# Optimization experiments

Measured on AMD Instinct MI355X. Metric: run time of the kernel, lower is better.

The kernel has to match this reference:

```python
import jax, jax.numpy as jnp
import numpy as np

B, S, NX, NH = 4, 1024, 1024, 16
HD = NX // NH  # 64


def setup_inputs() -> dict:
    key = jax.random.key(0)
    k1, k2, k3 = jax.random.split(key, 3)
    return {
        "hidden_states": jax.random.normal(k1, (B, S, NX), dtype=jnp.float32),
        "c_attn_w": jax.random.normal(k2, (NX, 3 * NX), dtype=jnp.float32) * 0.02,
        "c_attn_b": jnp.zeros((3 * NX,), dtype=jnp.float32),
        "c_proj_w": jax.random.normal(k3, (NX, NX), dtype=jnp.float32) * 0.02,
        "c_proj_b": jnp.zeros((NX,), dtype=jnp.float32),
    }


def reference(hidden_states, c_attn_w, c_attn_b, c_proj_w, c_proj_b):
    # Conv1D fused QKV projection: x @ W + b, then split into q,k,v
    qkv = hidden_states @ c_attn_w + c_attn_b  # [B,S,3*NX]
    q, k, v = jnp.split(qkv, 3, axis=-1)
    # split heads -> [B, H, S, D]
    def heads(x):
        return x.reshape(B, S, NH, HD).transpose(0, 2, 1, 3)
    q, k, v = heads(q), heads(k), heads(v)
    # scores: q @ k^T / sqrt(D)  (scale=True; NOTE: no causal mask in this fork)
    w = jnp.einsum("bhqd,bhkd->bhqk", q, k) / jnp.sqrt(jnp.asarray(HD, q.dtype))
    w = jax.nn.softmax(w, axis=-1)
    a = jnp.einsum("bhqk,bhkd->bhqd", w, v)  # [B,H,S,D]
    # merge heads -> [B,S,NX]
    a = a.transpose(0, 2, 1, 3).reshape(B, S, NX)
    # output projection (dropout is identity in eval)
    return a @ c_proj_w + c_proj_b
```

## Files before the change

### kernel.cpp

```cpp
#include <hip/hip_runtime.h>
#include <hip/hip_fp16.h>
#include <cmath>

constexpr int Bb  = 4;
constexpr int Ss  = 1024;
constexpr int NXc = 1024;
constexpr int NHc = 16;
constexpr int HDc = 64;

typedef __bf16    bf16x8 __attribute__((ext_vector_type(8)));
typedef _Float16  f16x8  __attribute__((ext_vector_type(8)));
typedef float     f32x4  __attribute__((ext_vector_type(4)));
typedef unsigned short ushortT;
typedef ushortT ushort8v __attribute__((ext_vector_type(8)));

#define QSCALE 0.18033688011112042f

__device__ __forceinline__ ushortT f2h_bits(float x) {
  return __half_as_ushort(__float2half(x));
}
__device__ __forceinline__ float h2f(ushortT h) {
  return __half2float(__ushort_as_half(h));
}
__device__ __forceinline__ void split_f16(float x, ushortT& hi, ushortT& lo) {
  hi = f2h_bits(x);
  lo = f2h_bits(x - h2f(hi));
}

__device__ __forceinline__ void gll16(const void* g, void* l) {
  __builtin_amdgcn_global_load_lds(
      (const __attribute__((address_space(1))) unsigned int*)g,
      (__attribute__((address_space(3))) unsigned int*)l, 16, 0, 0);
}

__device__ __forceinline__ void drain_vmem() {
  asm volatile("s_waitcnt vmcnt(0)" ::: "memory");
  __builtin_amdgcn_sched_barrier(0);
}

__global__ __launch_bounds__(256) void prep_all(
    const float* __restrict__ hs, const float* __restrict__ aw,
    const float* __restrict__ pw,
    ushortT* __restrict__ hF, ushortT* __restrict__ awT,
    ushortT* __restrict__ pwT)
{
  const int bid = blockIdx.x;
  if (bid < 4096) {
    int i = (bid * 256 + threadIdx.x) * 4;
    float4 v = *reinterpret_cast<const float4*>(&hs[i]);
    *reinterpret_cast<ushort4*>(&hF[i]) =
        make_ushort4(f2h_bits(v.x), f2h_bits(v.y), f2h_bits(v.z), f2h_bits(v.w));
    return;
  }
  __shared__ float tile[32][33];
  const int tx = threadIdx.x & 31, ty = threadIdx.x >> 5;
  if (bid < 7168) {
    const int b2 = bid - 4096;
    const int n0 = (b2 % 96) * 32, k0 = (b2 / 96) * 32;
    #pragma unroll
    for (int i = 0; i < 4; ++i)
      tile[ty + i * 8][tx] = aw[(size_t)(k0 + ty + i * 8) * 3072 + n0 + tx];
    __syncthreads();
    #pragma unroll
    for (int i = 0; i < 4; ++i)
      awT[(size_t)(n0 + ty + i * 8) * 1024 + k0 + tx] = f2h_bits(tile[tx][ty + i * 8]);
  } else {
    const int b2 = bid - 7168;
    const int n0 = (b2 & 31) * 32, k0 = (b2 >> 5) * 32;
    #pragma unroll
    for (int i = 0; i < 4; ++i)
      tile[ty + i * 8][tx] = pw[(size_t)(k0 + ty + i * 8) * 1024 + n0 + tx];
    __syncthreads();
    #pragma unroll
    for (int i = 0; i < 4; ++i)
      pwT[(size_t)(n0 + ty + i * 8) * 1024 + k0 + tx] = f2h_bits(tile[tx][ty + i * 8]);
  }
}

__global__ __launch_bounds__(256) void gemm_f16_qkv(
    const ushortT* __restrict__ A16, const ushortT* __restrict__ B16,
    const float* __restrict__ bias,
    ushortT* __restrict__ Qb, ushortT* __restrict__ Kb,
    ushortT* __restrict__ Vt, int M, int N, int K)
{
  constexpr int BK = 64;
  __shared__ ushortT smem[32768];

  const int t    = threadIdx.x;
  const int lane = t & 63;
  const int w    = t >> 6;
  const int wr   = w >> 1, wc = w & 1;
  const int m0 = blockIdx.y * 128;
  const int n0 = blockIdx.x * 128;
  const int l15 = lane & 15;
  const int g   = lane >> 4;

  const int srow  = w * 32 + (lane >> 3);
  const int sslot = (lane & 7) ^ (lane >> 3);

  f32x4 acc[4][4];
  #pragma unroll
  for (int m = 0; m < 4; ++m)
    #pragma unroll
    for (int n = 0; n < 4; ++n)
      #pragma unroll
      for (int r = 0; r < 4; ++r) acc[m][n][r] = 0.f;

  const ushortT* pA = A16 + (size_t)(m0 + srow) * K + sslot * 8;
  const ushortT* pB = B16 + (size_t)(n0 + srow) * K + sslot * 8;

  auto STAGE = [&](ushortT* buf, int k0) {
    #pragma unroll
    for (int i = 0; i < 4; ++i) {
      const size_t gstep = (size_t)i * 8 * K + k0;
      const int    loff  = (w * 32 + i * 8) * BK;
      gll16(pA + gstep, &buf[loff]);
      gll16(pB + gstep, &buf[8192 + loff]);
    }
  };

  const int arow = wr * 64 + l15;
  const int bcol = wc * 64 + l15;

  auto COMPUTE = [&](const ushortT* buf) {
    const ushortT* sA = buf;
    const ushortT* sB = buf + 8192;
    #pragma unroll
    for (int c = 0; c < 2; ++c) {
      const int slot = c * 4 + g;
      f16x8 af[4], bf[4];
      #pragma unroll
      for (int m = 0; m < 4; ++m) {
        int r   = arow + m * 16;
        int off = r * BK + ((slot ^ (r & 7)) * 8);
        af[m] = *reinterpret_cast<const f16x8*>(&sA[off]);
      }
      #pragma unroll
      for (int n = 0; n < 4; ++n) {
        int r   = bcol + n * 16;
        int off = r * BK + ((slot ^ (r & 7)) * 8);
        bf[n] = *reinterpret_cast<const f16x8*>(&sB[off]);
      }
      #pragma unroll
      for (int m = 0; m < 4; ++m)
        #pragma unroll
        for (int n = 0; n < 4; ++n)
          acc[m][n] = __builtin_amdgcn_mfma_f32_16x16x32_f16(af[m], bf[n], acc[m][n], 0, 0, 0);
    }
  };

  const int nt = K / BK;
  STAGE(&smem[0], 0);
  drain_vmem();
  __syncthreads();
  for (int tt = 0; tt < nt; tt += 2) {
    if (tt + 1 < nt) STAGE(&smem[16384], (tt + 1) * BK);
    COMPUTE(&smem[0]);
    drain_vmem();
    __syncthreads();
    if (tt + 2 < nt) STAGE(&smem[0], (tt + 2) * BK);
    COMPUTE(&smem[16384]);
    drain_vmem();
    __syncthreads();
  }

  const int region = n0 >> 10;
  if (region < 2) {
    #pragma unroll
    for (int n = 0; n < 4; ++n) {
      int col_g = n0 + wc * 64 + n * 16 + l15;
      int colm  = col_g & 1023;
      float bv  = bias[col_g];
      #pragma unroll
      for (int m = 0; m < 4; ++m) {
        int row = m0 + wr * 64 + m * 16 + (g << 2);
        #pragma unroll
        for (int r = 0; r < 4; ++r) {
          float v = acc[m][n][r] + bv;
          if (region == 0)
            Qb[(size_t)(row + r) * 1024 + colm] = f2h_bits(v * QSCALE);
          else
            Kb[(size_t)(row + r) * 1024 + colm] = f2h_bits(v);
        }
      }
    }
  } else {
    ushortT* T = smem;
    #pragma unroll
    for (int n = 0; n < 4; ++n) {
      int cl   = wc * 64 + n * 16 + l15;
      float bv = bias[n0 + cl];
      #pragma unroll
      for (int m = 0; m < 4; ++m) {
        int rl = wr * 64 + m * 16 + (g << 2);
        #pragma unroll
        for (int r = 0; r < 4; ++r)
          T[cl * 136 + rl + r] = f2h_bits(acc[m][n][r] + bv);
      }
    }
    __syncthreads();
    const int c  = t >> 1;
    const int rh = (t & 1) * 64;
    const int nn = (n0 - 2048) + c;
    const int hh = nn >> 6, dd = nn & 63;
    const int bb = m0 >> 10;
    const int sl = (m0 & 1023) + rh;
    size_t vbase = ((size_t)((bb * 16 + hh) * 64 + dd)) * 1024 + sl;
    #pragma unroll
    for (int j = 0; j < 8; ++j) {
      ushort8v v = *reinterpret_cast<const ushort8v*>(&T[c * 136 + rh + j * 8]);
      *reinterpret_cast<ushort8v*>(&Vt[vbase + j * 8]) = v;
    }
  }
}

__global__ __launch_bounds__(256) void gemm_f16p2(
    const ushortT* __restrict__ Ah, const ushortT* __restrict__ Al,
    const ushortT* __restrict__ B16,
    const float* __restrict__ bias, float* __restrict__ C,
    int M, int N, int K)
{
  constexpr int BK = 64;
  __shared__ ushortT smem[3 * 8192];
  ushortT* sAh = smem;
  ushortT* sAl = smem + 8192;
  ushortT* sB  = smem + 16384;

  const int t    = threadIdx.x;
  const int lane = t & 63;
  const int w    = t >> 6;
  const int wr   = w >> 1, wc = w & 1;
  const int m0 = blockIdx.y * 128;
  const int n0 = blockIdx.x * 128;
  const int l15 = lane & 15;
  const int g   = lane >> 4;

  const int srow  = w * 32 + (lane >> 3);
  const int sslot = (lane & 7) ^ (lane >> 3);

  f32x4 acc[4][4];
  #pragma unroll
  for (int m = 0; m < 4; ++m)
    #pragma unroll
    for (int n = 0; n < 4; ++n)
      #pragma unroll
      for (int r = 0; r < 4; ++r) acc[m][n][r] = 0.f;

  const ushortT* pAh = Ah  + (size_t)(m0 + srow) * K + sslot * 8;
  const ushortT* pAl = Al  + (size_t)(m0 + srow) * K + sslot * 8;
  const ushortT* pB  = B16 + (size_t)(n0 + srow) * K + sslot * 8;

  for (int k0 = 0; k0 < K; k0 += BK) {
    #pragma unroll
    for (int i = 0; i < 4; ++i) {
      const size_t gstep = (size_t)i * 8 * K + k0;
      const int    loff  = (w * 32 + i * 8) * BK;
      gll16(pAh + gstep, &sAh[loff]);
      gll16(pAl + gstep, &sAl[loff]);
      gll16(pB  + gstep, &sB[loff]);
    }
    __syncthreads();

    const int arow = wr * 64 + l15;
    const int bcol = wc * 64 + l15;
    #pragma unroll
    for (int c = 0; c < 2; ++c) {
      const int slot = c * 4 + g;
      f16x8 afh[4], afl[4], bf[4];
      #pragma unroll
      for (int m = 0; m < 4; ++m) {
        int r   = arow + m * 16;
        int off = r * BK + ((slot ^ (r & 7)) * 8);
        afh[m] = *reinterpret_cast<const f16x8*>(&sAh[off]);
        afl[m] = *reinterpret_cast<const f16x8*>(&sAl[off]);
      }
      #pragma unroll
      for (int n = 0; n < 4; ++n) {
        int r   = bcol + n * 16;
        int off = r * BK + ((slot ^ (r & 7)) * 8);
        bf[n] = *reinterpret_cast<const f16x8*>(&sB[off]);
      }
      #pragma unroll
      for (int m = 0; m < 4; ++m)
        #pragma unroll
        for (int n = 0; n < 4; ++n) {
          acc[m][n] = __builtin_amdgcn_mfma_f32_16x16x32_f16(afh[m], bf[n], acc[m][n], 0, 0, 0);
          acc[m][n] = __builtin_amdgcn_mfma_f32_16x16x32_f16(afl[m], bf[n], acc[m][n], 0, 0, 0);
        }
    }
    __syncthreads();
  }

  #pragma unroll
  for (int n = 0; n < 4; ++n) {
    int col  = n0 + wc * 64 + n * 16 + l15;
    float bv = bias[col];
    #pragma unroll
    for (int m = 0; m < 4; ++m) {
      int row = m0 + wr * 64 + m * 16 + (g << 2);
      #pragma unroll
      for (int r = 0; r < 4; ++r)
        C[(size_t)(row + r) * N + col] = acc[m][n][r] + bv;
    }
  }
}

__global__ __launch_bounds__(256) void attn_mfma(
    const ushortT* __restrict__ Qb, const ushortT* __restrict__ Kb,
    const ushortT* __restrict__ Vt,
    ushortT* __restrict__ aHi, ushortT* __restrict__ aLo)
{
  __shared__ ushortT sK[64 * 64];
  __shared__ ushortT sV[64 * 64];
  __shared__ ushortT sP[64 * 64];

  const int t    = threadIdx.x;
  const int lane = t & 63;
  const int w    = t >> 6;
  const int bh = blockIdx.x, b = bh >> 4, h = bh & 15;
  const int q0 = blockIdx.y * 64;
  const int l15 = lane & 15;
  const int g   = lane >> 4;

  f16x8 qa[2];
  #pragma unroll
  for (int ks = 0; ks < 2; ++ks) {
    size_t addr = (size_t)(b * 1024 + q0 + w * 16 + l15) * 1024
                  + h * 64 + ks * 32 + g * 8;
    qa[ks] = *reinterpret_cast<const f16x8*>(&Qb[addr]);
  }

  const int srow  = lane >> 3;
  const int sslot = (lane & 7) ^ srow;

  f32x4 O[4];
  float lp[4];
  #pragma unroll
  for (int r = 0; r < 4; ++r) lp[r] = 0.f;
  #pragma unroll
  for (int n = 0; n < 4; ++n)
    #pragma unroll
    for (int r = 0; r < 4; ++r) O[n][r] = 0.f;

  for (int kt = 0; kt < 16; ++kt) {
    const int k0 = kt * 64;
    #pragma unroll
    for (int i = 0; i < 2; ++i) {
      int r = w * 16 + i * 8 + srow;
      gll16(&Kb[(size_t)(b * 1024 + k0 + r) * 1024 + h * 64 + sslot * 8],
            &sK[(w * 16 + i * 8) * 64]);
      gll16(&Vt[((size_t)bh * 64 + r) * 1024 + k0 + sslot * 8],
            &sV[(w * 16 + i * 8) * 64]);
    }
    __syncthreads();

    f32x4 sc[4];
    #pragma unroll
    for (int n = 0; n < 4; ++n)
      #pragma unroll
      for (int r = 0; r < 4; ++r) sc[n][r] = 0.f;

    #pragma unroll
    for (int ks = 0; ks < 2; ++ks) {
      f16x8 kb[4];
      #pragma unroll
      for (int n = 0; n < 4; ++n) {
        int row = n * 16 + l15;
        kb[n] = *reinterpret_cast<const f16x8*>(
            &sK[row * 64 + (((g + ks * 4) ^ (row & 7)) * 8)]);
      }
      #pragma unroll
      for (int n = 0; n < 4; ++n)
        sc[n] = __builtin_amdgcn_mfma_f32_16x16x32_f16(qa[ks], kb[n], sc[n], 0, 0, 0);
    }

    #pragma unroll
    for (int n = 0; n < 4; ++n)
      #pragma unroll
      for (int r = 0; r < 4; ++r) {
        float p = exp2f(sc[n][r]);
        sc[n][r] = p;
        lp[r] += p;
      }

    #pragma unroll
    for (int n = 0; n < 4; ++n)
      #pragma unroll
      for (int r = 0; r < 4; ++r) {
        int prow = w * 16 + g * 4 + r;
        int c    = n * 16 + l15;
        int off2 = prow * 64 + ((((c >> 3) ^ (prow & 7)) << 3) | (c & 7));
        sP[off2] = f2h_bits(sc[n][r]);
      }

    #pragma unroll
    for (int ks = 0; ks < 2; ++ks) {
      f16x8 vb[4], pa;
      #pragma unroll
      for (int n = 0; n < 4; ++n) {
        int rd = n * 16 + l15;
        vb[n] = *reinterpret_cast<const f16x8*>(
            &sV[rd * 64 + (((g + ks * 4) ^ (rd & 7)) * 8)]);
      }
      {
        int pr = w * 16 + l15;
        pa = *reinterpret_cast<const f16x8*>(
            &sP[pr * 64 + (((g + ks * 4) ^ (pr & 7)) * 8)]);
      }
      #pragma unroll
      for (int n = 0; n < 4; ++n)
        O[n] = __builtin_amdgcn_mfma_f32_16x16x32_f16(pa, vb[n], O[n], 0, 0, 0);
    }
    __syncthreads();
  }

  #pragma unroll
  for (int off = 1; off < 16; off <<= 1)
    #pragma unroll
    for (int r = 0; r < 4; ++r)
      lp[r] += __shfl_xor(lp[r], off);

  #pragma unroll
  for (int r = 0; r < 4; ++r) {
    float inv = 1.f / lp[r];
    #pragma unroll
    for (int n = 0; n < 4; ++n) {
      ushortT hi, lo;
      split_f16(O[n][r] * inv, hi, lo);
      size_t off = (size_t)(b * 1024 + q0 + w * 16 + g * 4 + r) * 1024
                   + h * 64 + n * 16 + l15;
      aHi[off] = hi;
      aLo[off] = lo;
    }
  }
}

extern "C" void kernel_launch(void* const* d_in, const int* in_sizes, int n_in,
                              void* d_out, int out_size, void* d_ws, size_t ws_size,
                              hipStream_t stream) {
  const float* hs = (const float*)d_in[0];
  const float* aw = (const float*)d_in[1];
  const float* ab = (const float*)d_in[2];
  const float* pw = (const float*)d_in[3];
  const float* pb = (const float*)d_in[4];
  float* out = (float*)d_out;

  char* ws = (char*)d_ws;
  const int M = Bb * Ss;

  ushortT* hF  = (ushortT*)(ws);
  ushortT* awT = (ushortT*)(ws + ( 8u << 20));
  ushortT* pwT = (ushortT*)(ws + (14u << 20));
  ushortT* Qb  = (ushortT*)(ws + (18u << 20));
  ushortT* Kb  = (ushortT*)(ws + (26u << 20));
  ushortT* Vt  = (ushortT*)(ws + (34u << 20));
  ushortT* xHi = (ushortT*)(ws + (42u << 20));
  ushortT* xLo = (ushortT*)(ws + (50u << 20));

  dim3 blk(256);

  prep_all<<<8192, blk, 0, stream>>>(hs, aw, pw, hF, awT, pwT);
  gemm_f16_qkv<<<dim3(3 * NXc / 128, M / 128), blk, 0, stream>>>(
      hF, awT, ab, Qb, Kb, Vt, M, 3 * NXc, NXc);
  attn_mfma<<<dim3(Bb * NHc, Ss / 64), blk, 0, stream>>>(Qb, Kb, Vt, xHi, xLo);
  gemm_f16p2<<<dim3(NXc / 128, M / 128), blk, 0, stream>>>(
      xHi, xLo, pwT, pb, out, M, NXc, NXc);
}
```

Before: 119.2 us.

## Use single f16 attention output, double-buffer proj GEMM, MFMA row sums

The attention output is no longer split into hi/lo f16 pairs. The output projection GEMM now runs one MFMA per tile instead of two and reads half the A traffic. That GEMM also gains a two-stage LDS double buffer, so the next K-tile is fetched while the current one is computed. Softmax row sums are computed by an extra MFMA against a ones vector instead of scalar adds plus shuffles. The cost is lower precision in the projection input and more LDS per block.

```diff
diff --git a/kernel.cpp b/kernel.cpp
--- a/kernel.cpp
+++ b/kernel.cpp
@@ -18,13 +18,6 @@
 
 __device__ __forceinline__ ushortT f2h_bits(float x) {
   return __half_as_ushort(__float2half(x));
-}
-__device__ __forceinline__ float h2f(ushortT h) {
-  return __half2float(__ushort_as_half(h));
-}
-__device__ __forceinline__ void split_f16(float x, ushortT& hi, ushortT& lo) {
-  hi = f2h_bits(x);
-  lo = f2h_bits(x - h2f(hi));
 }
 
 __device__ __forceinline__ void gll16(const void* g, void* l) {
@@ -214,17 +207,13 @@
   }
 }
 
-__global__ __launch_bounds__(256) void gemm_f16p2(
-    const ushortT* __restrict__ Ah, const ushortT* __restrict__ Al,
-    const ushortT* __restrict__ B16,
+__global__ __launch_bounds__(256) void gemm_f16s(
+    const ushortT* __restrict__ A16, const ushortT* __restrict__ B16,
     const float* __restrict__ bias, float* __restrict__ C,
     int M, int N, int K)
 {
   constexpr int BK = 64;
-  __shared__ ushortT smem[3 * 8192];
-  ushortT* sAh = smem;
-  ushortT* sAl = smem + 8192;
-  ushortT* sB  = smem + 16384;
+  __shared__ ushortT smem[32768];
 
   const int t    = threadIdx.x;
   const int lane = t & 63;
@@ -246,33 +235,34 @@
       #pragma unroll
       for (int r = 0; r < 4; ++r) acc[m][n][r] = 0.f;
 
-  const ushortT* pAh = Ah  + (size_t)(m0 + srow) * K + sslot * 8;
-  const ushortT* pAl = Al  + (size_t)(m0 + srow) * K + sslot * 8;
-  const ushortT* pB  = B16 + (size_t)(n0 + srow) * K + sslot * 8;
-
-  for (int k0 = 0; k0 < K; k0 += BK) {
+  const ushortT* pA = A16 + (size_t)(m0 + srow) * K + sslot * 8;
+  const ushortT* pB = B16 + (size_t)(n0 + srow) * K + sslot * 8;
+
+  auto STAGE = [&](ushortT* buf, int k0) {
     #pragma unroll
     for (int i = 0; i < 4; ++i) {
       const size_t gstep = (size_t)i * 8 * K + k0;
       const int    loff  = (w * 32 + i * 8) * BK;
-      gll16(pAh + gstep, &sAh[loff]);
-      gll16(pAl + gstep, &sAl[loff]);
-      gll16(pB  + gstep, &sB[loff]);
-    }
-    __syncthreads();
-
-    const int arow = wr * 64 + l15;
-    const int bcol = wc * 64 + l15;
+      gll16(pA + gstep, &buf[loff]);
+      gll16(pB + gstep, &buf[8192 + loff]);
+    }
+  };
+
+  const int arow = wr * 64 + l15;
+  const int bcol = wc * 64 + l15;
+
+  auto COMPUTE = [&](const ushortT* buf) {
+    const ushortT* sA = buf;
+    const ushortT* sB = buf + 8192;
     #pragma unroll
     for (int c = 0; c < 2; ++c) {
       const int slot = c * 4 + g;
-      f16x8 afh[4], afl[4], bf[4];
+      f16x8 af[4], bf[4];
       #pragma unroll
       for (int m = 0; m < 4; ++m) {
         int r   = arow + m * 16;
         int off = r * BK + ((slot ^ (r & 7)) * 8);
-        afh[m] = *reinterpret_cast<const f16x8*>(&sAh[off]);
-        afl[m] = *reinterpret_cast<const f16x8*>(&sAl[off]);
+        af[m] = *reinterpret_cast<const f16x8*>(&sA[off]);
       }
       #pragma unroll
       for (int n = 0; n < 4; ++n) {
@@ -283,11 +273,23 @@
       #pragma unroll
       for (int m = 0; m < 4; ++m)
         #pragma unroll
-        for (int n = 0; n < 4; ++n) {
-          acc[m][n] = __builtin_amdgcn_mfma_f32_16x16x32_f16(afh[m], bf[n], acc[m][n], 0, 0, 0);
-          acc[m][n] = __builtin_amdgcn_mfma_f32_16x16x32_f16(afl[m], bf[n], acc[m][n], 0, 0, 0);
-        }
-    }
+        for (int n = 0; n < 4; ++n)
+          acc[m][n] = __builtin_amdgcn_mfma_f32_16x16x32_f16(af[m], bf[n], acc[m][n], 0, 0, 0);
+    }
+  };
+
+  const int nt = K / BK;
+  STAGE(&smem[0], 0);
+  drain_vmem();
+  __syncthreads();
+  for (int tt = 0; tt < nt; tt += 2) {
+    if (tt + 1 < nt) STAGE(&smem[16384], (tt + 1) * BK);
+    COMPUTE(&smem[0]);
+    drain_vmem();
+    __syncthreads();
+    if (tt + 2 < nt) STAGE(&smem[0], (tt + 2) * BK);
+    COMPUTE(&smem[16384]);
+    drain_vmem();
     __syncthreads();
   }
 
@@ -307,8 +309,7 @@
 
 __global__ __launch_bounds__(256) void attn_mfma(
     const ushortT* __restrict__ Qb, const ushortT* __restrict__ Kb,
-    const ushortT* __restrict__ Vt,
-    ushortT* __restrict__ aHi, ushortT* __restrict__ aLo)
+    const ushortT* __restrict__ Vt, ushortT* __restrict__ xF)
 {
   __shared__ ushortT sK[64 * 64];
   __shared__ ushortT sV[64 * 64];
@@ -330,13 +331,17 @@
     qa[ks] = *reinterpret_cast<const f16x8*>(&Qb[addr]);
   }
 
+  f16x8 ones;
+  #pragma unroll
+  for (int j = 0; j < 8; ++j) ones[j] = (_Float16)1.0f;
+
   const int srow  = lane >> 3;
   const int sslot = (lane & 7) ^ srow;
 
   f32x4 O[4];
-  float lp[4];
-  #pragma unroll
-  for (int r = 0; r < 4; ++r) lp[r] = 0.f;
+  f32x4 lO;
+  #pragma unroll
+  for (int r = 0; r < 4; ++r) lO[r] = 0.f;
   #pragma unroll
   for (int n = 0; n < 4; ++n)
     #pragma unroll
@@ -377,11 +382,8 @@
     #pragma unroll
     for (int n = 0; n < 4; ++n)
       #pragma unroll
-      for (int r = 0; r < 4; ++r) {
-        float p = exp2f(sc[n][r]);
-        sc[n][r] = p;
-        lp[r] += p;
-      }
+      for (int r = 0; r < 4; ++r)
+        sc[n][r] = exp2f(sc[n][r]);
 
     #pragma unroll
     for (int n = 0; n < 4; ++n)
@@ -410,27 +412,19 @@
       #pragma unroll
       for (int n = 0; n < 4; ++n)
         O[n] = __builtin_amdgcn_mfma_f32_16x16x32_f16(pa, vb[n], O[n], 0, 0, 0);
-    }
-    __syncthreads();
-  }
-
-  #pragma unroll
-  for (int off = 1; off < 16; off <<= 1)
-    #pragma unroll
-    for (int r = 0; r < 4; ++r)
-      lp[r] += __shfl_xor(lp[r], off);
+      lO = __builtin_amdgcn_mfma_f32_16x16x32_f16(pa, ones, lO, 0, 0, 0);
+    }
+    __syncthreads();
+  }
 
   #pragma unroll
   for (int r = 0; r < 4; ++r) {
-    float inv = 1.f / lp[r];
+    float inv = 1.f / lO[r];
     #pragma unroll
     for (int n = 0; n < 4; ++n) {
-      ushortT hi, lo;
-      split_f16(O[n][r] * inv, hi, lo);
       size_t off = (size_t)(b * 1024 + q0 + w * 16 + g * 4 + r) * 1024
                    + h * 64 + n * 16 + l15;
-      aHi[off] = hi;
-      aLo[off] = lo;
+      xF[off] = f2h_bits(O[n][r] * inv);
     }
   }
 }
@@ -454,15 +448,14 @@
   ushortT* Qb  = (ushortT*)(ws + (18u << 20));
   ushortT* Kb  = (ushortT*)(ws + (26u << 20));
   ushortT* Vt  = (ushortT*)(ws + (34u << 20));
-  ushortT* xHi = (ushortT*)(ws + (42u << 20));
-  ushortT* xLo = (ushortT*)(ws + (50u << 20));
+  ushortT* xF  = (ushortT*)(ws + (42u << 20));
 
   dim3 blk(256);
 
   prep_all<<<8192, blk, 0, stream>>>(hs, aw, pw, hF, awT, pwT);
   gemm_f16_qkv<<<dim3(3 * NXc / 128, M / 128), blk, 0, stream>>>(
       hF, awT, ab, Qb, Kb, Vt, M, 3 * NXc, NXc);
-  attn_mfma<<<dim3(Bb * NHc, Ss / 64), blk, 0, stream>>>(Qb, Kb, Vt, xHi, xLo);
-  gemm_f16p2<<<dim3(NXc / 128, M / 128), blk, 0, stream>>>(
-      xHi, xLo, pwT, pb, out, M, NXc, NXc);
-}
+  attn_mfma<<<dim3(Bb * NHc, Ss / 64), blk, 0, stream>>>(Qb, Kb, Vt, xF);
+  gemm_f16s<<<dim3(NXc / 128, M / 128), blk, 0, stream>>>(
+      xF, pwT, pb, out, M, NXc, NXc);
+}
```

Result: faster. 100.5 us (-15.7%).
